# Kernel tuning notes

Measured on AMD Instinct MI355X. Metric: run time of the kernel, lower is better.

Reference implementation:

```python
import jax, jax.numpy as jnp
import numpy as np

JITTER = 0.05  # posterior-covariance jitter (constructor arg `jitter`)
TWO_PI = 2.0 * np.pi


def _local_k(x1, x2, ls, std):
    # 1-D RBF kernel: x1 (A,), x2 (B,) -> (A, B)
    d2 = jnp.square(x1[:, None] - x2[None, :])
    return (std * std) * jnp.exp(-0.5 * d2 / (ls * ls))


def setup_inputs() -> dict:
    key = jax.random.key(0)
    ks = jax.random.split(key, 8)
    N, D, M = 3072, 4, 512
    X = jax.random.normal(ks[0], (N, D), dtype=jnp.float32)
    y = jax.random.normal(ks[1], (N, 1), dtype=jnp.float32)
    X_bar = jax.random.normal(ks[2], (M, D), dtype=jnp.float32)
    # learned parameters (moderate positive values so fp32 Choleskys are stable)
    local_gp_ls = 1.0 + 0.1 * jax.random.normal(ks[3], (D,), dtype=jnp.float32)
    local_gp_std = 0.5 + 0.05 * jax.random.normal(ks[4], (D,), dtype=jnp.float32)
    local_gp_noise_std = 0.3 * jnp.ones((D,), dtype=jnp.float32)
    local_ls = 0.3 + 0.5 * jax.random.uniform(ks[5], (M, D), dtype=jnp.float32)
    global_gp_std = jnp.array([0.7], dtype=jnp.float32)
    global_gp_noise_std = jnp.array([0.5], dtype=jnp.float32)
    return {
        "X": X, "y": y, "X_bar": X_bar,
        "local_gp_ls": local_gp_ls, "local_gp_std": local_gp_std,
        "local_gp_noise_std": local_gp_noise_std, "local_ls": local_ls,
        "global_gp_std": global_gp_std, "global_gp_noise_std": global_gp_noise_std,
    }


def reference(X, y, X_bar, local_gp_ls, local_gp_std, local_gp_noise_std,
              local_ls, global_gp_std, global_gp_noise_std):
    # NSGP.nlml() in training mode.
    N, D = X.shape
    M = X_bar.shape[0]
    dtype = X.dtype
    eyeM = jnp.eye(M, dtype=dtype)
    eyeN = jnp.eye(N, dtype=dtype)
    log_lbar = jnp.log(jnp.abs(local_ls))  # (M, D)

    def per_dim(xb, xd, ls, std, noise, loglb):
        # local GP over inducing points for one input dimension
        k = _local_k(xb, xb, ls, std) + (noise * noise) * eyeM  # (M, M)
        c = jnp.linalg.cholesky(k)
        alpha = jax.scipy.linalg.cho_solve((c, True), loglb[:, None])  # (M, 1)
        kstar = _local_k(xd, xb, ls, std)  # (N, M)
        l = jnp.exp(kstar @ alpha)[:, 0]   # (N,) predicted lengthscales
        kss = _local_k(xd, xd, ls, std)    # (N, N)
        v = jax.scipy.linalg.cho_solve((c, True), kstar.T)  # (M, N)
        kpost = kss - kstar @ v + JITTER * eyeN             # posterior cov
        pc = jnp.linalg.cholesky(kpost)
        Bd = jnp.sum(jnp.log(jnp.diagonal(pc)))
        return l, Bd

    # batch the per-dimension local-GP work across the D input dims
    l_dn, B_d = jax.vmap(per_dim, in_axes=(1, 1, 0, 0, 0, 1))(
        X_bar, X, local_gp_ls, local_gp_std, local_gp_noise_std, log_lbar)
    l = l_dn.T  # (N, D)

    # nonstationary global kernel (Gibbs kernel)
    l1 = l[:, None, :]                    # (N, 1, D)
    l2 = l[None, :, :]                    # (1, N, D)
    lsq = l1 * l1 + l2 * l2               # (N, N, D)
    suffix = jnp.prod(jnp.sqrt(2.0 * l1 * l2 / lsq), axis=2)  # (N, N)
    d2 = jnp.square(X[:, None, :] - X[None, :, :])            # (N, N, D)
    gvar = global_gp_std[0] * global_gp_std[0]
    K = gvar * suffix * jnp.exp(-jnp.sum(d2 / lsq, axis=2))
    K = K + (global_gp_noise_std[0] ** 2) * eyeN

    L = jnp.linalg.cholesky(K)
    alpha = jax.scipy.linalg.cho_solve((L, True), y)  # (N, 1)
    log2pi = jnp.log(jnp.asarray(TWO_PI, dtype))
    A = 0.5 * ((y.T @ alpha)[0, 0]
               + jnp.sum(jnp.log(jnp.diagonal(L)))
               + N * log2pi)
    B = jnp.sum(B_d) + 0.5 * (M * D * log2pi)
    return A + B
```

## Files before the change

kernel.cpp:

```cpp
#include <hip/hip_runtime.h>
#include <math.h>

#define N_   3072
#define D_   4
#define M_   512
#define NPAD 3200
#define NB   128
#define PW   32
#define NBLK (NPAD/NB)
#define MBLK (M_/NB)
#define JITTER_ 0.05f
#define CBORD 32768.0f
#define LTS  132

__device__ void trsm_tile64(float* A, int lda, int row0, int k0, const float* Tinv,
                            float* As, float* Ts, int lt) {
  const int tx = lt & 15, ty = lt >> 4;
  float acc[4][8];
  #pragma unroll
  for (int i = 0; i < 4; ++i)
    #pragma unroll
    for (int u = 0; u < 8; ++u) acc[i][u] = 0.f;
  for (int ks = 0; ks < NB; ks += 32) {
    for (int t = lt; t < 64*8; t += 256) {
      int r = t >> 3, q = t & 7;
      float4 v = *(const float4*)&A[(size_t)(row0 + r)*lda + k0 + ks + q*4];
      As[(q*4+0)*68 + r] = v.x; As[(q*4+1)*68 + r] = v.y;
      As[(q*4+2)*68 + r] = v.z; As[(q*4+3)*68 + r] = v.w;
    }
    for (int t = lt; t < 128*8; t += 256) {
      int c = t >> 3, q = t & 7;
      float4 v = *(const float4*)&Tinv[c*NB + ks + q*4];
      Ts[(q*4+0)*132 + c] = v.x; Ts[(q*4+1)*132 + c] = v.y;
      Ts[(q*4+2)*132 + c] = v.z; Ts[(q*4+3)*132 + c] = v.w;
    }
    __syncthreads();
    #pragma unroll
    for (int kk = 0; kk < 32; ++kk) {
      float a[4], b[8];
      *(float4*)a      = *(const float4*)&As[kk*68 + ty*4];
      *(float4*)&b[0]  = *(const float4*)&Ts[kk*132 + tx*8];
      *(float4*)&b[4]  = *(const float4*)&Ts[kk*132 + tx*8 + 4];
      #pragma unroll
      for (int i = 0; i < 4; ++i)
        #pragma unroll
        for (int u = 0; u < 8; ++u) acc[i][u] += a[i]*b[u];
    }
    __syncthreads();
  }
  #pragma unroll
  for (int i = 0; i < 4; ++i) {
    size_t off = (size_t)(row0 + ty*4 + i)*lda + k0 + tx*8;
    *(float4*)&A[off]     = make_float4(acc[i][0],acc[i][1],acc[i][2],acc[i][3]);
    *(float4*)&A[off + 4] = make_float4(acc[i][4],acc[i][5],acc[i][6],acc[i][7]);
  }
}

__device__ void presub64(const float* A, int lda, int j0, int p0, int sr, int sc,
                         int valid, float* As, float* Bs, float* LT_, int lt) {
  const int tx = lt & 15, ty = lt >> 4;
  float acc[4][4];
  #pragma unroll
  for (int i=0;i<4;++i){acc[i][0]=0.f;acc[i][1]=0.f;acc[i][2]=0.f;acc[i][3]=0.f;}
  for (int ks = 0; ks < NB; ks += 32) {
    __syncthreads();
    if (valid) {
      for (int t = lt; t < 64*8; t += 256) {
        int rr = t >> 3, qq = t & 7;
        float4 v = *(const float4*)&A[(size_t)(j0+sr*64+rr)*lda + p0 + ks + qq*4];
        As[(qq*4+0)*68+rr]=v.x; As[(qq*4+1)*68+rr]=v.y;
        As[(qq*4+2)*68+rr]=v.z; As[(qq*4+3)*68+rr]=v.w;
        float4 w = *(const float4*)&A[(size_t)(j0+sc*64+rr)*lda + p0 + ks + qq*4];
        Bs[(qq*4+0)*68+rr]=w.x; Bs[(qq*4+1)*68+rr]=w.y;
        Bs[(qq*4+2)*68+rr]=w.z; Bs[(qq*4+3)*68+rr]=w.w;
      }
    }
    __syncthreads();
    if (valid) {
      #pragma unroll
      for (int kk = 0; kk < 32; ++kk) {
        float a[4], b[4];
        *(float4*)a = *(const float4*)&As[kk*68 + ty*4];
        *(float4*)b = *(const float4*)&Bs[kk*68 + tx*4];
        #pragma unroll
        for (int i=0;i<4;++i)
          #pragma unroll
          for (int u=0;u<4;++u) acc[i][u] += a[i]*b[u];
      }
    }
  }
  if (valid) {
    #pragma unroll
    for (int i=0;i<4;++i)
      #pragma unroll
      for (int u=0;u<4;++u) {
        int rr = sr*64 + ty*4 + i, cc = sc*64 + tx*4 + u;
        if (cc <= rr) LT_[cc*LTS + rr] -= acc[i][u];
      }
  }
}

__device__ void potrf_duty(float* A, int lda, int b, int presub, int doInv,
                           float* Tinv, float* logsum, int slot, int limit,
                           float* LT_, float* SM_, float* pivd_) {
  const int tid = threadIdx.x;
  const int j0 = b * NB;
  for (int t = tid; t < NB*NB; t += 512) {
    int r = t >> 7, c = t & 127;
    float v = 0.f;
    if (c <= r) v = A[(size_t)(j0+r)*lda + (j0+c)];
    LT_[c*LTS + r] = v;
  }
  if (presub) {
    int half = tid >> 8, lt = tid & 255;
    float* As = SM_ + half*4352; float* Bs = As + 2176;
    const int p0 = j0 - NB;
    presub64(A, lda, j0, p0, half, 0, 1, As, Bs, LT_, lt);
    presub64(A, lda, j0, p0, 1, 1, half==0 ? 1 : 0, As, Bs, LT_, lt);
  }
  __syncthreads();
  #pragma unroll
  for (int p = 0; p < 4; ++p) {
    const int pc0 = p*PW, pc1 = pc0 + PW;
    for (int j = pc0; j < pc1; ++j) {
      float dd = fmaxf(LT_[j*LTS + j], 1e-30f);
      if (tid == 0) pivd_[j] = dd;
      float rd = 1.0f / dd;
      int wn = pc1 - 1 - j;
      for (int t = tid; t < wn*NB; t += 512) {
        int c = j + 1 + (t >> 7);
        int i = t & 127;
        if (i >= c) LT_[c*LTS + i] -= LT_[j*LTS + i] * LT_[j*LTS + c] * rd;
      }
      __syncthreads();
    }
    for (int t = tid; t < PW*NB; t += 512) {
      int jc = pc0 + (t >> 7);
      int i  = t & 127;
      float dd = pivd_[jc];
      if (i > jc)       LT_[jc*LTS + i] *= rsqrtf(dd);
      else if (i == jc) LT_[jc*LTS + i] = sqrtf(dd);
    }
    __syncthreads();
    if (pc1 < NB) {
      const int rem = NB - pc1, g4 = rem >> 2;
      for (int t = tid; t < g4*g4; t += 512) {
        int tr = t / g4, tc = t - tr*g4;
        if (tc > tr) continue;
        int i0 = pc1 + tr*4, c0 = pc1 + tc*4;
        float acc2[4][4];
        #pragma unroll
        for (int i=0;i<4;++i){acc2[i][0]=0.f;acc2[i][1]=0.f;acc2[i][2]=0.f;acc2[i][3]=0.f;}
        #pragma unroll
        for (int jj = 0; jj < PW; ++jj) {
          float av[4], bv[4];
          *(float4*)av = *(const float4*)&LT_[(pc0+jj)*LTS + i0];
          *(float4*)bv = *(const float4*)&LT_[(pc0+jj)*LTS + c0];
          #pragma unroll
          for (int i=0;i<4;++i)
            #pragma unroll
            for (int u=0;u<4;++u) acc2[i][u] += av[i]*bv[u];
        }
        #pragma unroll
        for (int i=0;i<4;++i)
          #pragma unroll
          for (int u=0;u<4;++u) {
            int rr = i0+i, cc = c0+u;
            if (cc <= rr) LT_[cc*LTS + rr] -= acc2[i][u];
          }
      }
      __syncthreads();
    }
  }
  for (int t = tid; t < NB*NB; t += 512) {
    int r = t >> 7, c = t & 127;
    if (c <= r) A[(size_t)(j0+r)*lda + (j0+c)] = LT_[c*LTS + r];
  }
  {
    float lg = 0.f;
    if (tid < NB) {
      int g = j0 + tid;
      if (g < limit) lg = 0.5f * logf(pivd_[tid]);
    }
    for (int o = 32; o; o >>= 1) lg += __shfl_down(lg, o);
    int wv = tid >> 6;
    if ((tid & 63) == 0 && wv < 2) logsum[slot*2 + wv] = lg;
  }
  if (!doInv) return;
  float* Wp = SM_;
  float* Tt = SM_ + 10240;
  for (int t = tid; t < 4*1024; t += 512) {
    int I = t >> 10, e = t & 1023;
    int r = e >> 5, c = e & 31;
    Wp[(I*(I+1)/2 + I)*1024 + e] = (r == c) ? 1.f : 0.f;
  }
  __syncthreads();
  {
    int wI = tid >> 7;
    int lane = tid & 127;
    float* Rb = &Wp[(wI*(wI+1)/2 + wI)*1024];
    for (int j = 0; j < 32; ++j) {
      float dinv = 1.0f / LT_[(wI*32+j)*LTS + (wI*32+j)];
      for (int t = lane; t < 1024; t += 128) {
        int i = t >> 5, c = t & 31;
        if (i > j && c <= j)
          Rb[i*32 + c] -= LT_[(wI*32+j)*LTS + (wI*32+i)] * Rb[j*32 + c] * dinv;
      }
      __syncthreads();
    }
    for (int t = lane; t < 1024; t += 128) {
      int i = t >> 5, c = t & 31;
      if (c <= i) Rb[i*32 + c] *= 1.0f / LT_[(wI*32+i)*LTS + (wI*32+i)];
    }
    __syncthreads();
  }
  #pragma unroll
  for (int dist = 1; dist < 4; ++dist) {
    const int nb = 4 - dist;
    for (int t = tid; t < nb*1024; t += 512) {
      int bb = t >> 10, e = t & 1023;
      int r = e >> 5, c = e & 31;
      int J = bb, I = bb + dist;
      float s = 0.f;
      for (int K = J; K < I; ++K) {
        const float* Wkj = &Wp[(K*(K+1)/2 + J)*1024];
        #pragma unroll
        for (int k = 0; k < 32; ++k)
          s += LT_[(K*32+k)*LTS + (I*32+r)] * Wkj[k*32 + c];
      }
      Tt[bb*1024 + e] = s;
    }
    __syncthreads();
    for (int t = tid; t < nb*1024; t += 512) {
      int bb = t >> 10, e = t & 1023;
      int r = e >> 5, c = e & 31;
      int J = bb, I = bb + dist;
      const float* Wii = &Wp[(I*(I+1)/2 + I)*1024];
      float s = 0.f;
      #pragma unroll
      for (int k = 0; k < 32; ++k)
        s += Wii[r*32 + k] * Tt[bb*1024 + k*32 + c];
      Wp[(I*(I+1)/2 + J)*1024 + e] = -s;
    }
    __syncthreads();
  }
  for (int t = tid; t < NB*32; t += 512) {
    int i = t >> 5, c4 = (t & 31) * 4;
    int I = i >> 5, J = c4 >> 5;
    float4 v;
    if (J <= I) {
      const float* Wij = &Wp[(I*(I+1)/2 + J)*1024 + (i & 31)*32 + (c4 & 31)];
      v = *(const float4*)Wij;
    } else v = make_float4(0.f, 0.f, 0.f, 0.f);
    *(float4*)&Tinv[i*NB + c4] = v;
  }
}

__global__ __launch_bounds__(512, 1)
void k_panel(float* Abase, size_t aStride, int lda, int k, int init, int doInv,
             float* TinvBase, size_t tz, size_t tk,
             float* logsum, int slotBase, int limit, int nblk) {
  __shared__ __align__(16) float LT[128*LTS];
  __shared__ __align__(16) float SM[13312];
  __shared__ float pivd[NB];
  const int z = blockIdx.z;
  float* A = Abase + (size_t)z*aStride;
  float* Tz = TinvBase + (size_t)z*tz;
  const int tid = threadIdx.x;

  if (init) {
    if (blockIdx.x == 0)
      potrf_duty(A, lda, 0, 0, doInv, Tz, logsum, slotBase + z*32, limit,
                 LT, SM, pivd);
    return;
  }
  const int m = nblk - 1 - k;
  const float* TinvK = Tz + (size_t)k*tk;
  int half = tid >> 8, lt = tid & 255;
  float* As = SM + half*6400;
  float* Ts = As + 2176;

  if (blockIdx.x == 0) {
    trsm_tile64(A, lda, (k+1)*NB + half*64, k*NB, TinvK, As, Ts, lt);
    __syncthreads();
    potrf_duty(A, lda, k+1, 1, doInv, Tz + (size_t)(k+1)*tk,
               logsum, slotBase + z*32 + (k+1), limit, LT, SM, pivd);
  } else {
    int t = 2 + (blockIdx.x - 1)*2 + half;
    if (t < 2*m)
      trsm_tile64(A, lda, (k+1)*NB + t*64, k*NB, TinvK, As, Ts, lt);
  }
}

__global__ __launch_bounds__(256)
void k_syrk(float* Abase, size_t aStride, int lda, int kblk) {
  if (blockIdx.y > blockIdx.x) return;
  if (blockIdx.x < 2 && blockIdx.y < 2) return;
  __shared__ float As[32*68];
  __shared__ float Bs[32*68];
  const int tid = threadIdx.x;
  float* A = Abase + (size_t)blockIdx.z * aStride;
  const int k0 = kblk * NB;
  const int row0 = k0 + NB + blockIdx.x * 64;
  const int col0 = k0 + NB + blockIdx.y * 64;
  const int tx = tid & 15, ty = tid >> 4;
  float acc[4][4];
  #pragma unroll
  for (int i=0;i<4;++i) { acc[i][0]=0.f;acc[i][1]=0.f;acc[i][2]=0.f;acc[i][3]=0.f; }
  for (int ks = 0; ks < NB; ks += 32) {
    for (int t = tid; t < 64*8; t += 256) {
      int r = t >> 3, q = t & 7;
      float4 v = *(const float4*)&A[(size_t)(row0 + r)*lda + k0 + ks + q*4];
      As[(q*4+0)*68 + r] = v.x; As[(q*4+1)*68 + r] = v.y;
      As[(q*4+2)*68 + r] = v.z; As[(q*4+3)*68 + r] = v.w;
      float4 w = *(const float4*)&A[(size_t)(col0 + r)*lda + k0 + ks + q*4];
      Bs[(q*4+0)*68 + r] = w.x; Bs[(q*4+1)*68 + r] = w.y;
      Bs[(q*4+2)*68 + r] = w.z; Bs[(q*4+3)*68 + r] = w.w;
    }
    __syncthreads();
    #pragma unroll
    for (int kk = 0; kk < 32; ++kk) {
      float a[4], b[4];
      *(float4*)a = *(const float4*)&As[kk*68 + ty*4];
      *(float4*)b = *(const float4*)&Bs[kk*68 + tx*4];
      #pragma unroll
      for (int i=0;i<4;++i)
        #pragma unroll
        for (int u=0;u<4;++u) acc[i][u] += a[i]*b[u];
    }
    __syncthreads();
  }
  #pragma unroll
  for (int i=0;i<4;++i) {
    size_t off = (size_t)(row0 + ty*4 + i)*lda + col0 + tx*4;
    float4 v = *(const float4*)&A[off];
    v.x -= acc[i][0]; v.y -= acc[i][1]; v.z -= acc[i][2]; v.w -= acc[i][3];
    *(float4*)&A[off] = v;
  }
}

__global__ __launch_bounds__(256)
void k_build_kb(const float* Xbar, const float* lsp, const float* stdp, const float* noisep,
                float* KbBase, size_t kbStride, int dimBase) {
  int z = blockIdx.z, d = dimBase + z;
  float* Kb = KbBase + (size_t)z*kbStride;
  int idx = blockIdx.x*256 + threadIdx.x;
  if (idx >= M_*M_) return;
  int i = idx >> 9, j = idx & 511;
  float ls = lsp[d], sd = stdp[d], nz = noisep[d];
  float df = Xbar[i*D_ + d] - Xbar[j*D_ + d];
  float v = sd*sd*expf(-0.5f*df*df/(ls*ls));
  if (i == j) v += nz*nz;
  Kb[idx] = v;
}

__global__ __launch_bounds__(256)
void k_build_kstar(const float* X, const float* Xbar, const float* lsp, const float* stdp,
                   float* KSBase, size_t ksStride, int dimBase) {
  int z = blockIdx.z, d = dimBase + z;
  float* KS = KSBase + (size_t)z*ksStride;
  int idx = blockIdx.x*256 + threadIdx.x;
  if (idx >= N_*M_) return;
  int i = idx >> 9, j = idx & 511;
  float ls = lsp[d], sd = stdp[d];
  float df = X[i*D_ + d] - Xbar[j*D_ + d];
  KS[idx] = sd*sd*expf(-0.5f*df*df/(ls*ls));
}

__global__ __launch_bounds__(256)
void k_csolve(float* CBase, size_t cStride, const float* KbBase, size_t kbStride,
              const float* TinvKbBase, size_t tkbStride, int J) {
  __shared__ float sm[12672];
  const int tid = threadIdx.x;
  float* C = CBase + (size_t)blockIdx.z*cStride;
  const float* L = KbBase + (size_t)blockIdx.z*kbStride;
  const float* Tinv = TinvKbBase + (size_t)blockIdx.z*tkbStride + (size_t)J*NB*NB;
  const int row0 = blockIdx.x*64;
  const int tx = tid & 15, ty = tid >> 4;
  float* As = sm; float* Ls = sm + 2176;
  float* Xs = sm; float* Ts = sm + 8448;
  float acc[4][8];
  #pragma unroll
  for (int i=0;i<4;++i) {
    const float* p = &C[(size_t)(row0+ty*4+i)*M_ + J*NB + tx*8];
    float4 v0 = *(const float4*)p, v1 = *(const float4*)(p+4);
    acc[i][0]=v0.x; acc[i][1]=v0.y; acc[i][2]=v0.z; acc[i][3]=v0.w;
    acc[i][4]=v1.x; acc[i][5]=v1.y; acc[i][6]=v1.z; acc[i][7]=v1.w;
  }
  for (int P = 0; P < J; ++P) {
    for (int ks = 0; ks < NB; ks += 32) {
      __syncthreads();
      for (int t = tid; t < 64*8; t += 256) {
        int r = t >> 3, q = t & 7;
        float4 v = *(const float4*)&C[(size_t)(row0+r)*M_ + P*NB + ks + q*4];
        As[(q*4+0)*68+r]=v.x; As[(q*4+1)*68+r]=v.y; As[(q*4+2)*68+r]=v.z; As[(q*4+3)*68+r]=v.w;
      }
      for (int t = tid; t < 128*8; t += 256) {
        int c = t >> 3, q = t & 7;
        float4 v = *(const float4*)&L[(size_t)(J*NB+c)*M_ + P*NB + ks + q*4];
        Ls[(q*4+0)*132+c]=v.x; Ls[(q*4+1)*132+c]=v.y; Ls[(q*4+2)*132+c]=v.z; Ls[(q*4+3)*132+c]=v.w;
      }
      __syncthreads();
      #pragma unroll
      for (int kk = 0; kk < 32; ++kk) {
        float a[4], b[8];
        *(float4*)a     = *(const float4*)&As[kk*68 + ty*4];
        *(float4*)&b[0] = *(const float4*)&Ls[kk*132 + tx*8];
        *(float4*)&b[4] = *(const float4*)&Ls[kk*132 + tx*8 + 4];
        #pragma unroll
        for (int i=0;i<4;++i)
          #pragma unroll
          for (int u=0;u<8;++u) acc[i][u] -= a[i]*b[u];
      }
    }
  }
  __syncthreads();
  #pragma unroll
  for (int i=0;i<4;++i)
    #pragma unroll
    for (int u=0;u<8;++u) Xs[(ty*4+i)*132 + tx*8+u] = acc[i][u];
  #pragma unroll
  for (int i=0;i<4;++i)
    #pragma unroll
    for (int u=0;u<8;++u) acc[i][u] = 0.f;
  for (int ms = 0; ms < NB; ms += 32) {
    for (int t = tid; t < 128*8; t += 256) {
      int c = t >> 3, q = t & 7;
      float4 v = *(const float4*)&Tinv[c*NB + ms + q*4];
      Ts[(q*4+0)*132+c]=v.x; Ts[(q*4+1)*132+c]=v.y; Ts[(q*4+2)*132+c]=v.z; Ts[(q*4+3)*132+c]=v.w;
    }
    __syncthreads();
    #pragma unroll
    for (int mm = 0; mm < 32; ++mm) {
      float a[4], b[8];
      a[0]=Xs[(ty*4+0)*132+ms+mm]; a[1]=Xs[(ty*4+1)*132+ms+mm];
      a[2]=Xs[(ty*4+2)*132+ms+mm]; a[3]=Xs[(ty*4+3)*132+ms+mm];
      *(float4*)&b[0] = *(const float4*)&Ts[mm*132 + tx*8];
      *(float4*)&b[4] = *(const float4*)&Ts[mm*132 + tx*8 + 4];
      #pragma unroll
      for (int i=0;i<4;++i)
        #pragma unroll
        for (int u=0;u<8;++u) acc[i][u] += a[i]*b[u];
    }
    __syncthreads();
  }
  #pragma unroll
  for (int i=0;i<4;++i) {
    float* p = &C[(size_t)(row0+ty*4+i)*M_ + J*NB + tx*8];
    *(float4*)p     = make_float4(acc[i][0],acc[i][1],acc[i][2],acc[i][3]);
    *(float4*)(p+4) = make_float4(acc[i][4],acc[i][5],acc[i][6],acc[i][7]);
  }
}

__global__ __launch_bounds__(256)
void k_fwdsub(const float* KbBase, size_t kbStride,
              const float* TkbBase, size_t tkbStride,
              const float* lls, float* wBase, size_t wStride, int dimBase) {
  __shared__ float w[M_];
  __shared__ float tv[NB];
  __shared__ float red[256];
  int z = blockIdx.z, d = dimBase + z;
  const float* L = KbBase + (size_t)z*kbStride;
  const float* Tk = TkbBase + (size_t)z*tkbStride;
  float* wout = wBase + (size_t)z*wStride;
  const int tid = threadIdx.x;
  for (int i = tid; i < M_; i += 256) w[i] = logf(fabsf(lls[i*D_ + d]));
  __syncthreads();
  const int r = tid >> 1, h = tid & 1;
  for (int J = 0; J < 4; ++J) {
    float s = 0.f;
    int half = (J*NB) >> 1;
    for (int k = h*half; k < (h+1)*half; k += 4) {
      float4 lv = *(const float4*)&L[(size_t)(J*NB + r)*M_ + k];
      s += lv.x*w[k] + lv.y*w[k+1] + lv.z*w[k+2] + lv.w*w[k+3];
    }
    red[tid] = s;
    __syncthreads();
    if (h == 0) tv[r] = w[J*NB + r] - red[2*r] - red[2*r+1];
    __syncthreads();
    const float* Ti = Tk + (size_t)J*NB*NB;
    s = 0.f;
    for (int k = h*64; k < h*64 + 64; k += 4) {
      float4 tw = *(const float4*)&Ti[r*NB + k];
      s += tw.x*tv[k] + tw.y*tv[k+1] + tw.z*tv[k+2] + tw.w*tv[k+3];
    }
    red[tid] = s;
    __syncthreads();
    if (h == 0) w[J*NB + r] = red[2*r] + red[2*r+1];
    __syncthreads();
  }
  for (int i = tid; i < M_; i += 256) wout[i] = w[i];
}

__global__ __launch_bounds__(256)
void k_gemv_l(const float* CBase, size_t cStride, const float* wBase, size_t wStride,
              float* lvec, int dimBase) {
  int z = blockIdx.z, d = dimBase + z;
  const float* C = CBase + (size_t)z*cStride;
  const float* w = wBase + (size_t)z*wStride;
  __shared__ float ws[M_];
  for (int i = threadIdx.x; i < M_; i += 256) ws[i] = w[i];
  __syncthreads();
  int wid = threadIdx.x >> 6, lane = threadIdx.x & 63;
  int row = blockIdx.x*4 + wid;
  if (row >= N_) return;
  float s = 0.f;
  const float* cr = &C[(size_t)row*M_];
  for (int k = lane; k < M_; k += 64) s += cr[k]*ws[k];
  for (int o = 32; o; o >>= 1) s += __shfl_down(s, o);
  if (lane == 0) lvec[row*D_ + d] = expf(s);
}

__global__ __launch_bounds__(256)
void k_kpost(const float* X, const float* lsp, const float* stdp,
             const float* CBase, size_t cStride,
             float* Abase, size_t aStride, int dimBase) {
  if (blockIdx.y > blockIdx.x) return;
  __shared__ float As[32*68];
  __shared__ float Bs[32*68];
  int z = blockIdx.z, d = dimBase + z;
  const float* C = CBase + (size_t)z*cStride;
  float* A = Abase + (size_t)z*aStride;
  const int row0 = blockIdx.x*64, col0 = blockIdx.y*64;
  const int tid = threadIdx.x, tx = tid & 15, ty = tid >> 4;
  float acc[4][4];
  #pragma unroll
  for (int i=0;i<4;++i) { acc[i][0]=0.f;acc[i][1]=0.f;acc[i][2]=0.f;acc[i][3]=0.f; }
  if (row0 < N_) {
    for (int ks = 0; ks < M_; ks += 32) {
      for (int t = tid; t < 64*8; t += 256) {
        int r = t >> 3, q = t & 7;
        float4 v = *(const float4*)&C[(size_t)(row0+r)*M_ + ks + q*4];
        As[(q*4+0)*68+r]=v.x; As[(q*4+1)*68+r]=v.y; As[(q*4+2)*68+r]=v.z; As[(q*4+3)*68+r]=v.w;
        float4 w2 = *(const float4*)&C[(size_t)(col0+r)*M_ + ks + q*4];
        Bs[(q*4+0)*68+r]=w2.x; Bs[(q*4+1)*68+r]=w2.y; Bs[(q*4+2)*68+r]=w2.z; Bs[(q*4+3)*68+r]=w2.w;
      }
      __syncthreads();
      #pragma unroll
      for (int kk=0; kk<32; ++kk) {
        float a[4], b[4];
        *(float4*)a = *(const float4*)&As[kk*68 + ty*4];
        *(float4*)b = *(const float4*)&Bs[kk*68 + tx*4];
        #pragma unroll
        for (int i=0;i<4;++i)
          #pragma unroll
          for (int u=0;u<4;++u) acc[i][u] += a[i]*b[u];
      }
      __syncthreads();
    }
  }
  float ls = lsp[d], sd = stdp[d];
  float inv2 = -0.5f/(ls*ls), s2 = sd*sd;
  #pragma unroll
  for (int i=0;i<4;++i) {
    int gi = row0 + ty*4 + i;
    float xi = (gi < N_) ? X[gi*D_ + d] : 0.f;
    #pragma unroll
    for (int u=0;u<4;++u) {
      int gj = col0 + tx*4 + u;
      float v;
      if (gi < N_ && gj < N_) {
        float df = xi - X[gj*D_ + d];
        v = s2*expf(inv2*df*df) - acc[i][u];
        if (gi == gj) v += JITTER_;
      } else {
        v = (gi == gj) ? 1.f : 0.f;
      }
      A[(size_t)gi*NPAD + gj] = v;
    }
  }
}

__global__ __launch_bounds__(256)
void k_kfinal(const float* X, const float* lvec, const float* y,
              const float* gstd, const float* gnoise, float* A) {
  int idx = blockIdx.x*256 + threadIdx.x;
  if (idx >= NPAD*NPAD) return;
  int gi = idx / NPAD, gj = idx - (idx/NPAD)*NPAD;
  float v;
  if (gi < N_ && gj < N_) {
    float gv = gstd[0]*gstd[0];
    float prod = 1.f, s = 0.f;
    #pragma unroll
    for (int d = 0; d < D_; ++d) {
      float l1 = lvec[gi*D_ + d], l2 = lvec[gj*D_ + d];
      float lsq = l1*l1 + l2*l2;
      prod *= 2.f*l1*l2/lsq;
      float df = X[gi*D_ + d] - X[gj*D_ + d];
      s += df*df/lsq;
    }
    v = gv * sqrtf(prod) * expf(-s);
    if (gi == gj) v += gnoise[0]*gnoise[0];
  } else if (gi == N_ && gj < N_) v = y[gj];
  else if (gj == N_ && gi < N_) v = y[gi];
  else if (gi == N_ && gj == N_) v = CBORD;
  else v = (gi == gj) ? 1.f : 0.f;
  A[idx] = v;
}

__global__ void k_finalize(const float* A, const float* logsum, float* out) {
  if (threadIdx.x != 0 || blockIdx.x != 0) return;
  float sumB = 0.f;
  for (int z = 0; z < 4; ++z)
    for (int k = 0; k < NBLK; ++k) {
      int slot = z*32 + k;
      sumB += logsum[slot*2] + logsum[slot*2+1];
    }
  float sumL = 0.f;
  for (int k = 0; k < NBLK; ++k) {
    int slot = 128 + k;
    sumL += logsum[slot*2] + logsum[slot*2+1];
  }
  float lb = A[(size_t)N_*NPAD + N_];
  float yKy = CBORD - lb*lb;
  const float LOG2PI = 1.8378770664093453f;
  float Aterm = 0.5f*(yKy + sumL + (float)N_*LOG2PI);
  float Bterm = sumB + 0.5f*(float)(M_*D_)*LOG2PI;
  out[0] = Aterm + Bterm;
}

static void run_chain(float* A, size_t aS, int lda, int nblk,
                      float* Tinv, size_t tz, size_t tk, int invAll,
                      float* lgs, int slotBase, int limit, int nz,
                      hipStream_t stream) {
  int doInv0 = (invAll || nblk > 1) ? 1 : 0;
  k_panel<<<dim3(1,1,nz),512,0,stream>>>(A,aS,lda, 0,1,doInv0, Tinv,tz,tk,
                                         lgs,slotBase,limit, nblk);
  for (int k = 0; k < nblk-1; ++k) {
    int m = nblk-1-k;
    int doInv = (invAll || (k+1 < nblk-1)) ? 1 : 0;
    k_panel<<<dim3(m,1,nz),512,0,stream>>>(A,aS,lda, k,0,doInv, Tinv,tz,tk,
                                           lgs,slotBase,limit, nblk);
    if (m >= 2)
      k_syrk<<<dim3(2*m,2*m,nz),256,0,stream>>>(A,aS,lda,k);
  }
}

extern "C" void kernel_launch(void* const* d_in, const int* in_sizes, int n_in,
                              void* d_out, int out_size, void* d_ws, size_t ws_size,
                              hipStream_t stream) {
  const float* X    = (const float*)d_in[0];
  const float* y    = (const float*)d_in[1];
  const float* Xbar = (const float*)d_in[2];
  const float* lgls = (const float*)d_in[3];
  const float* lgstd= (const float*)d_in[4];
  const float* lgnz = (const float*)d_in[5];
  const float* lls  = (const float*)d_in[6];
  const float* gstd = (const float*)d_in[7];
  const float* gnz  = (const float*)d_in[8];
  float* out = (float*)d_out;

  const size_t A_SZ   = (size_t)NPAD*NPAD;
  const size_t KS_SZ  = (size_t)N_*M_;
  const size_t KB_SZ  = (size_t)M_*M_;
  const size_t TKB_SZ = (size_t)MBLK*NB*NB;
  const size_t TBG_SZ = (size_t)NBLK*NB*NB;
  const size_t W_SZ   = (size_t)M_;
  const size_t LV_SZ  = (size_t)N_*D_;
  const size_t LOG_SZ = 1024;

  size_t need2 = (5*A_SZ + 4*(KS_SZ + KB_SZ + TKB_SZ + W_SZ) + 5*TBG_SZ
                  + LV_SZ + LOG_SZ + 1024);
  size_t per1  = A_SZ + KS_SZ + KB_SZ + TKB_SZ + TBG_SZ + W_SZ;
  size_t need1 = 4*per1 + LV_SZ + LOG_SZ + 256;

  if (ws_size >= need2 * sizeof(float)) {
    float* p = (float*)d_ws;
    float* A    = p; p += 5*A_SZ;
    float* KS   = p; p += 4*KS_SZ;
    float* Kb   = p; p += 4*KB_SZ;
    float* Tkb  = p; p += 4*TKB_SZ;
    float* Tbig = p; p += 5*TBG_SZ;
    float* wv   = p; p += 4*W_SZ;
    float* lv   = p; p += LV_SZ;
    float* lgs  = p; p += LOG_SZ;

    k_build_kb<<<dim3((M_*M_+255)/256,1,4),256,0,stream>>>(Xbar,lgls,lgstd,lgnz,Kb,KB_SZ,0);
    run_chain(Kb, KB_SZ, M_, MBLK, Tkb, TKB_SZ, (size_t)NB*NB, 1, lgs, 192, 0, 4, stream);
    k_fwdsub<<<dim3(1,1,4),256,0,stream>>>(Kb,KB_SZ,Tkb,TKB_SZ,lls,wv,W_SZ,0);
    k_build_kstar<<<dim3((N_*M_+255)/256,1,4),256,0,stream>>>(X,Xbar,lgls,lgstd,KS,KS_SZ,0);
    for (int J = 0; J < MBLK; ++J)
      k_csolve<<<dim3(N_/64,1,4),256,0,stream>>>(KS,KS_SZ,Kb,KB_SZ,Tkb,TKB_SZ,J);
    k_gemv_l<<<dim3(N_/4,1,4),256,0,stream>>>(KS,KS_SZ,wv,W_SZ,lv,0);
    k_kpost<<<dim3(NPAD/64,NPAD/64,4),256,0,stream>>>(X,lgls,lgstd,KS,KS_SZ,A,A_SZ,0);
    k_kfinal<<<dim3((NPAD*NPAD+255)/256,1,1),256,0,stream>>>(X,lv,y,gstd,gnz,A+4*A_SZ);
    run_chain(A, A_SZ, NPAD, NBLK, Tbig, TBG_SZ, (size_t)NB*NB, 0, lgs, 0, N_, 5, stream);
    k_finalize<<<1,64,0,stream>>>(A+4*A_SZ,lgs,out);
    return;
  }

  bool batched = ws_size >= need1 * sizeof(float);
  int nz = batched ? 4 : 1;
  float* p = (float*)d_ws;
  float* A    = p; p += (size_t)nz*A_SZ;
  float* KS   = p; p += (size_t)nz*KS_SZ;
  float* Kb   = p; p += (size_t)nz*KB_SZ;
  float* Tkb  = p; p += (size_t)nz*TKB_SZ;
  float* Tbig = p; p += (size_t)nz*TBG_SZ;
  float* wv   = p; p += (size_t)nz*W_SZ;
  float* lv   = p; p += LV_SZ;
  float* lgs  = p; p += LOG_SZ;

  int npass = batched ? 1 : 4;
  for (int pass = 0; pass < npass; ++pass) {
    int dimBase  = batched ? 0 : pass;
    int slotBase = batched ? 0 : pass*32;
    k_build_kb<<<dim3((M_*M_+255)/256,1,nz),256,0,stream>>>(Xbar,lgls,lgstd,lgnz,Kb,KB_SZ,dimBase);
    run_chain(Kb, KB_SZ, M_, MBLK, Tkb, TKB_SZ, (size_t)NB*NB, 1, lgs, 192+slotBase, 0, nz, stream);
    k_fwdsub<<<dim3(1,1,nz),256,0,stream>>>(Kb,KB_SZ,Tkb,TKB_SZ,lls,wv,W_SZ,dimBase);
    k_build_kstar<<<dim3((N_*M_+255)/256,1,nz),256,0,stream>>>(X,Xbar,lgls,lgstd,KS,KS_SZ,dimBase);
    for (int J = 0; J < MBLK; ++J)
      k_csolve<<<dim3(N_/64,1,nz),256,0,stream>>>(KS,KS_SZ,Kb,KB_SZ,Tkb,TKB_SZ,J);
    k_gemv_l<<<dim3(N_/4,1,nz),256,0,stream>>>(KS,KS_SZ,wv,W_SZ,lv,dimBase);
    k_kpost<<<dim3(NPAD/64,NPAD/64,nz),256,0,stream>>>(X,lgls,lgstd,KS,KS_SZ,A,A_SZ,dimBase);
    run_chain(A, A_SZ, NPAD, NBLK, Tbig, TBG_SZ, (size_t)NB*NB, 0, lgs, slotBase, N_, nz, stream);
  }
  k_kfinal<<<dim3((NPAD*NPAD+255)/256,1,1),256,0,stream>>>(X,lv,y,gstd,gnz,A);
  run_chain(A, A_SZ, NPAD, NBLK, Tbig, TBG_SZ, (size_t)NB*NB, 0, lgs, 128, N_, 1, stream);
  k_finalize<<<1,64,0,stream>>>(A,lgs,out);
}
```

Baseline: 8.684 ms.

## Fuse panel and trailing SYRK into one lookahead kernel per Cholesky step

Restructures the blocked Cholesky so that each step launches a single combined kernel instead of separate panel and SYRK launches. Block 0 applies the deferred trailing update from the previous step to the next panel, runs its TRSM and factors the diagonal block. The other blocks handle the remaining TRSM tiles and the lagged SYRK tiles, which cuts launches per step and overlaps the critical-path factorization with the bulk update. The diagonal factor now works from a smaller shared-memory strip with 256 threads, reading and writing global memory directly. That trades the large LDS footprint for more global traffic on the serial path, and the triangular-index decode and lagged-update bookkeeping add correctness risk.

```diff
diff --git a/kernel.cpp b/kernel.cpp
--- a/kernel.cpp
+++ b/kernel.cpp
@@ -6,12 +6,48 @@
 #define M_   512
 #define NPAD 3200
 #define NB   128
-#define PW   32
 #define NBLK (NPAD/NB)
 #define MBLK (M_/NB)
 #define JITTER_ 0.05f
 #define CBORD 32768.0f
-#define LTS  132
+
+__device__ void syrk64(float* A, int lda, int gr0, int gc0, int k0,
+                       float* As, float* Bs, int lt) {
+  const int tx = lt & 15, ty = lt >> 4;
+  float acc[4][4];
+  #pragma unroll
+  for (int i=0;i<4;++i){acc[i][0]=0.f;acc[i][1]=0.f;acc[i][2]=0.f;acc[i][3]=0.f;}
+  for (int ks = 0; ks < NB; ks += 32) {
+    __syncthreads();
+    for (int t = lt; t < 64*8; t += 256) {
+      int rr = t >> 3, qq = t & 7;
+      float4 v = *(const float4*)&A[(size_t)(gr0+rr)*lda + k0 + ks + qq*4];
+      As[(qq*4+0)*68+rr]=v.x; As[(qq*4+1)*68+rr]=v.y;
+      As[(qq*4+2)*68+rr]=v.z; As[(qq*4+3)*68+rr]=v.w;
+      float4 w = *(const float4*)&A[(size_t)(gc0+rr)*lda + k0 + ks + qq*4];
+      Bs[(qq*4+0)*68+rr]=w.x; Bs[(qq*4+1)*68+rr]=w.y;
+      Bs[(qq*4+2)*68+rr]=w.z; Bs[(qq*4+3)*68+rr]=w.w;
+    }
+    __syncthreads();
+    #pragma unroll
+    for (int kk = 0; kk < 32; ++kk) {
+      float a[4], b[4];
+      *(float4*)a = *(const float4*)&As[kk*68 + ty*4];
+      *(float4*)b = *(const float4*)&Bs[kk*68 + tx*4];
+      #pragma unroll
+      for (int i=0;i<4;++i)
+        #pragma unroll
+        for (int u=0;u<4;++u) acc[i][u] += a[i]*b[u];
+    }
+  }
+  #pragma unroll
+  for (int i=0;i<4;++i) {
+    size_t off = (size_t)(gr0 + ty*4 + i)*lda + gc0 + tx*4;
+    float4 v = *(const float4*)&A[off];
+    v.x -= acc[i][0]; v.y -= acc[i][1]; v.z -= acc[i][2]; v.w -= acc[i][3];
+    *(float4*)&A[off] = v;
+  }
+}
 
 __device__ void trsm_tile64(float* A, int lda, int row0, int k0, const float* Tinv,
                             float* As, float* Ts, int lt) {
@@ -56,287 +92,218 @@
   }
 }
 
-__device__ void presub64(const float* A, int lda, int j0, int p0, int sr, int sc,
-                         int valid, float* As, float* Bs, float* LT_, int lt) {
-  const int tx = lt & 15, ty = lt >> 4;
-  float acc[4][4];
-  #pragma unroll
-  for (int i=0;i<4;++i){acc[i][0]=0.f;acc[i][1]=0.f;acc[i][2]=0.f;acc[i][3]=0.f;}
-  for (int ks = 0; ks < NB; ks += 32) {
-    __syncthreads();
-    if (valid) {
-      for (int t = lt; t < 64*8; t += 256) {
-        int rr = t >> 3, qq = t & 7;
-        float4 v = *(const float4*)&A[(size_t)(j0+sr*64+rr)*lda + p0 + ks + qq*4];
-        As[(qq*4+0)*68+rr]=v.x; As[(qq*4+1)*68+rr]=v.y;
-        As[(qq*4+2)*68+rr]=v.z; As[(qq*4+3)*68+rr]=v.w;
-        float4 w = *(const float4*)&A[(size_t)(j0+sc*64+rr)*lda + p0 + ks + qq*4];
-        Bs[(qq*4+0)*68+rr]=w.x; Bs[(qq*4+1)*68+rr]=w.y;
-        Bs[(qq*4+2)*68+rr]=w.z; Bs[(qq*4+3)*68+rr]=w.w;
-      }
-    }
-    __syncthreads();
-    if (valid) {
-      #pragma unroll
-      for (int kk = 0; kk < 32; ++kk) {
-        float a[4], b[4];
-        *(float4*)a = *(const float4*)&As[kk*68 + ty*4];
-        *(float4*)b = *(const float4*)&Bs[kk*68 + tx*4];
-        #pragma unroll
-        for (int i=0;i<4;++i)
-          #pragma unroll
-          for (int u=0;u<4;++u) acc[i][u] += a[i]*b[u];
-      }
-    }
-  }
-  if (valid) {
-    #pragma unroll
-    for (int i=0;i<4;++i)
-      #pragma unroll
-      for (int u=0;u<4;++u) {
-        int rr = sr*64 + ty*4 + i, cc = sc*64 + tx*4 + u;
-        if (cc <= rr) LT_[cc*LTS + rr] -= acc[i][u];
-      }
-  }
-}
-
-__device__ void potrf_duty(float* A, int lda, int b, int presub, int doInv,
-                           float* Tinv, float* logsum, int slot, int limit,
-                           float* LT_, float* SM_, float* pivd_) {
+__device__ void b_potrf_l2(float* A, int lda, int dj, float* Tinv, int doInv,
+                           float* logsum, int slot, int limit,
+                           float* SM, float* diagv) {
   const int tid = threadIdx.x;
-  const int j0 = b * NB;
-  for (int t = tid; t < NB*NB; t += 512) {
-    int r = t >> 7, c = t & 127;
-    float v = 0.f;
-    if (c <= r) v = A[(size_t)(j0+r)*lda + (j0+c)];
-    LT_[c*LTS + r] = v;
-  }
-  if (presub) {
-    int half = tid >> 8, lt = tid & 255;
-    float* As = SM_ + half*4352; float* Bs = As + 2176;
-    const int p0 = j0 - NB;
-    presub64(A, lda, j0, p0, half, 0, 1, As, Bs, LT_, lt);
-    presub64(A, lda, j0, p0, 1, 1, half==0 ? 1 : 0, As, Bs, LT_, lt);
-  }
-  __syncthreads();
+  float* Ps = SM;
   #pragma unroll
   for (int p = 0; p < 4; ++p) {
-    const int pc0 = p*PW, pc1 = pc0 + PW;
-    for (int j = pc0; j < pc1; ++j) {
-      float dd = fmaxf(LT_[j*LTS + j], 1e-30f);
-      if (tid == 0) pivd_[j] = dd;
-      float rd = 1.0f / dd;
-      int wn = pc1 - 1 - j;
-      for (int t = tid; t < wn*NB; t += 512) {
-        int c = j + 1 + (t >> 7);
-        int i = t & 127;
-        if (i >= c) LT_[c*LTS + i] -= LT_[j*LTS + i] * LT_[j*LTS + c] * rd;
-      }
-      __syncthreads();
-    }
-    for (int t = tid; t < PW*NB; t += 512) {
-      int jc = pc0 + (t >> 7);
-      int i  = t & 127;
-      float dd = pivd_[jc];
-      if (i > jc)       LT_[jc*LTS + i] *= rsqrtf(dd);
-      else if (i == jc) LT_[jc*LTS + i] = sqrtf(dd);
-    }
-    __syncthreads();
-    if (pc1 < NB) {
-      const int rem = NB - pc1, g4 = rem >> 2;
-      for (int t = tid; t < g4*g4; t += 512) {
+    const int pc0 = p*32;
+    const int nr = NB - pc0;
+    __syncthreads();
+    for (int t = tid; t < nr*32; t += 256) {
+      int r2 = t >> 5, c2 = t & 31;
+      Ps[r2*33 + c2] = A[(size_t)(dj+pc0+r2)*lda + dj+pc0+c2];
+    }
+    __syncthreads();
+    for (int j = 0; j < 32; ++j) {
+      if (tid == 0) {
+        float piv = sqrtf(fmaxf(Ps[j*33+j], 1e-30f));
+        Ps[j*33+j] = piv;
+        diagv[pc0+j] = piv;
+      }
+      __syncthreads();
+      float ip = 1.0f / Ps[j*33+j];
+      for (int t = tid; t < nr-1-j; t += 256)
+        Ps[(j+1+t)*33 + j] *= ip;
+      __syncthreads();
+      int rw = nr-1-j, cw = 31-j;
+      for (int t = tid; t < rw*cw; t += 256) {
+        int rr = t / cw, cc2 = t - rr*cw;
+        int i = j+1+rr, c2 = j+1+cc2;
+        Ps[i*33 + c2] -= Ps[i*33 + j] * Ps[c2*33 + j];
+      }
+      __syncthreads();
+    }
+    for (int t = tid; t < nr*32; t += 256) {
+      int r2 = t >> 5, c2 = t & 31;
+      if (r2 >= c2)
+        A[(size_t)(dj+pc0+r2)*lda + dj+pc0+c2] = Ps[r2*33 + c2];
+    }
+    __syncthreads();
+    if (p < 3) {
+      int rem = nr - 32;
+      int g4 = rem >> 2;
+      for (int t = tid; t < g4*g4; t += 256) {
         int tr = t / g4, tc = t - tr*g4;
         if (tc > tr) continue;
-        int i0 = pc1 + tr*4, c0 = pc1 + tc*4;
-        float acc2[4][4];
-        #pragma unroll
-        for (int i=0;i<4;++i){acc2[i][0]=0.f;acc2[i][1]=0.f;acc2[i][2]=0.f;acc2[i][3]=0.f;}
-        #pragma unroll
-        for (int jj = 0; jj < PW; ++jj) {
+        int i0 = 32 + tr*4, c0 = 32 + tc*4;
+        float acc[4][4];
+        #pragma unroll
+        for (int i=0;i<4;++i){acc[i][0]=0.f;acc[i][1]=0.f;acc[i][2]=0.f;acc[i][3]=0.f;}
+        #pragma unroll
+        for (int jj = 0; jj < 32; ++jj) {
           float av[4], bv[4];
-          *(float4*)av = *(const float4*)&LT_[(pc0+jj)*LTS + i0];
-          *(float4*)bv = *(const float4*)&LT_[(pc0+jj)*LTS + c0];
+          #pragma unroll
+          for (int x=0;x<4;++x) { av[x] = Ps[(i0+x)*33+jj]; bv[x] = Ps[(c0+x)*33+jj]; }
           #pragma unroll
           for (int i=0;i<4;++i)
             #pragma unroll
-            for (int u=0;u<4;++u) acc2[i][u] += av[i]*bv[u];
+            for (int u=0;u<4;++u) acc[i][u] += av[i]*bv[u];
         }
         #pragma unroll
         for (int i=0;i<4;++i)
           #pragma unroll
           for (int u=0;u<4;++u) {
             int rr = i0+i, cc = c0+u;
-            if (cc <= rr) LT_[cc*LTS + rr] -= acc2[i][u];
+            if (cc <= rr)
+              A[(size_t)(dj+pc0+rr)*lda + dj+pc0+cc] -= acc[i][u];
           }
       }
       __syncthreads();
     }
-  }
-  for (int t = tid; t < NB*NB; t += 512) {
-    int r = t >> 7, c = t & 127;
-    if (c <= r) A[(size_t)(j0+r)*lda + (j0+c)] = LT_[c*LTS + r];
   }
   {
     float lg = 0.f;
     if (tid < NB) {
-      int g = j0 + tid;
-      if (g < limit) lg = 0.5f * logf(pivd_[tid]);
+      int g = dj + tid;
+      if (g < limit) lg = logf(diagv[tid]);
     }
     for (int o = 32; o; o >>= 1) lg += __shfl_down(lg, o);
     int wv = tid >> 6;
     if ((tid & 63) == 0 && wv < 2) logsum[slot*2 + wv] = lg;
   }
   if (!doInv) return;
-  float* Wp = SM_;
-  float* Tt = SM_ + 10240;
-  for (int t = tid; t < 4*1024; t += 512) {
-    int I = t >> 10, e = t & 1023;
-    int r = e >> 5, c = e & 31;
-    Wp[(I*(I+1)/2 + I)*1024 + e] = (r == c) ? 1.f : 0.f;
-  }
+  float* Wd = SM;
+  float* Tt = SM + 4224;
   __syncthreads();
   {
-    int wI = tid >> 7;
-    int lane = tid & 127;
-    float* Rb = &Wp[(wI*(wI+1)/2 + wI)*1024];
+    int w = tid >> 6, lane = tid & 63;
+    float* R = Wd + w*1056;
+    for (int t = lane; t < 1024; t += 64) {
+      int i=t>>5, c2=t&31; R[i*33+c2] = (i==c2)?1.f:0.f;
+    }
+    __syncthreads();
     for (int j = 0; j < 32; ++j) {
-      float dinv = 1.0f / LT_[(wI*32+j)*LTS + (wI*32+j)];
-      for (int t = lane; t < 1024; t += 128) {
-        int i = t >> 5, c = t & 31;
-        if (i > j && c <= j)
-          Rb[i*32 + c] -= LT_[(wI*32+j)*LTS + (wI*32+i)] * Rb[j*32 + c] * dinv;
-      }
-      __syncthreads();
-    }
-    for (int t = lane; t < 1024; t += 128) {
-      int i = t >> 5, c = t & 31;
-      if (c <= i) Rb[i*32 + c] *= 1.0f / LT_[(wI*32+i)*LTS + (wI*32+i)];
-    }
-    __syncthreads();
-  }
-  #pragma unroll
-  for (int dist = 1; dist < 4; ++dist) {
-    const int nb = 4 - dist;
-    for (int t = tid; t < nb*1024; t += 512) {
-      int bb = t >> 10, e = t & 1023;
-      int r = e >> 5, c = e & 31;
-      int J = bb, I = bb + dist;
-      float s = 0.f;
-      for (int K = J; K < I; ++K) {
-        const float* Wkj = &Wp[(K*(K+1)/2 + J)*1024];
-        #pragma unroll
-        for (int k = 0; k < 32; ++k)
-          s += LT_[(K*32+k)*LTS + (I*32+r)] * Wkj[k*32 + c];
-      }
-      Tt[bb*1024 + e] = s;
-    }
-    __syncthreads();
-    for (int t = tid; t < nb*1024; t += 512) {
-      int bb = t >> 10, e = t & 1023;
-      int r = e >> 5, c = e & 31;
-      int J = bb, I = bb + dist;
-      const float* Wii = &Wp[(I*(I+1)/2 + I)*1024];
-      float s = 0.f;
-      #pragma unroll
-      for (int k = 0; k < 32; ++k)
-        s += Wii[r*32 + k] * Tt[bb*1024 + k*32 + c];
-      Wp[(I*(I+1)/2 + J)*1024 + e] = -s;
-    }
-    __syncthreads();
-  }
-  for (int t = tid; t < NB*32; t += 512) {
-    int i = t >> 5, c4 = (t & 31) * 4;
-    int I = i >> 5, J = c4 >> 5;
-    float4 v;
-    if (J <= I) {
-      const float* Wij = &Wp[(I*(I+1)/2 + J)*1024 + (i & 31)*32 + (c4 & 31)];
-      v = *(const float4*)Wij;
-    } else v = make_float4(0.f, 0.f, 0.f, 0.f);
-    *(float4*)&Tinv[i*NB + c4] = v;
-  }
-}
-
-__global__ __launch_bounds__(512, 1)
-void k_panel(float* Abase, size_t aStride, int lda, int k, int init, int doInv,
+      float dinv = 1.0f / A[(size_t)(dj+w*32+j)*lda + dj+w*32+j];
+      for (int t = lane; t < 1024; t += 64) {
+        int i = t>>5, c2 = t&31;
+        if (i > j && c2 <= j)
+          R[i*33+c2] -= A[(size_t)(dj+w*32+i)*lda + dj+w*32+j] * R[j*33+c2] * dinv;
+      }
+      __syncthreads();
+    }
+    for (int t = lane; t < 1024; t += 64) {
+      int i=t>>5, c2=t&31;
+      if (c2 <= i) R[i*33+c2] *= 1.0f / A[(size_t)(dj+w*32+i)*lda + dj+w*32+i];
+    }
+    __syncthreads();
+  }
+  for (int t = tid; t < NB*NB; t += 256) {
+    int i = t >> 7, c2 = t & 127;
+    int I = i >> 5, J = c2 >> 5;
+    float v = 0.f;
+    if (I == J) v = Wd[I*1056 + (i&31)*33 + (c2&31)];
+    Tinv[i*NB + c2] = v;
+  }
+  __syncthreads();
+  for (int d = 1; d < 4; ++d) {
+    for (int J = 0; J + d < 4; ++J) {
+      int I = J + d;
+      for (int t = tid; t < 1024; t += 256) {
+        int r2 = t >> 5, c2 = t & 31;
+        float s = 0.f;
+        for (int K = J; K < I; ++K) {
+          const float* Arow = &A[(size_t)(dj+I*32+r2)*lda + dj + K*32];
+          const float* Wcol = &Tinv[(size_t)(K*32)*NB + J*32 + c2];
+          #pragma unroll
+          for (int kk2 = 0; kk2 < 32; ++kk2)
+            s += Arow[kk2] * Wcol[(size_t)kk2*NB];
+        }
+        Tt[r2*33 + c2] = s;
+      }
+      __syncthreads();
+      for (int t = tid; t < 1024; t += 256) {
+        int r2 = t >> 5, c2 = t & 31;
+        float s = 0.f;
+        #pragma unroll
+        for (int kk2 = 0; kk2 < 32; ++kk2)
+          s += Wd[I*1056 + r2*33 + kk2] * Tt[kk2*33 + c2];
+        Tinv[(size_t)(I*32+r2)*NB + J*32 + c2] = -s;
+      }
+      __syncthreads();
+    }
+  }
+}
+
+__global__ __launch_bounds__(256)
+void k_init(float* Abase, size_t aStride, int lda, float* TinvBase, size_t tz,
+            float* logsum, int slotBase, int limit, int doInv) {
+  __shared__ __align__(16) float SM[6528];
+  __shared__ float diagv[NB];
+  int z = blockIdx.z;
+  b_potrf_l2(Abase + (size_t)z*aStride, lda, 0, TinvBase + (size_t)z*tz, doInv,
+             logsum, slotBase + z*32, limit, SM, diagv);
+}
+
+__global__ __launch_bounds__(256)
+void k_combo(float* Abase, size_t aStride, int lda, int k, int doInv,
              float* TinvBase, size_t tz, size_t tk,
-             float* logsum, int slotBase, int limit, int nblk) {
-  __shared__ __align__(16) float LT[128*LTS];
-  __shared__ __align__(16) float SM[13312];
-  __shared__ float pivd[NB];
+             float* logsum, int slotBase, int limit, int nP) {
+  __shared__ __align__(16) float SM[6528];
+  __shared__ float diagv[NB];
   const int z = blockIdx.z;
   float* A = Abase + (size_t)z*aStride;
   float* Tz = TinvBase + (size_t)z*tz;
   const int tid = threadIdx.x;
-
-  if (init) {
-    if (blockIdx.x == 0)
-      potrf_duty(A, lda, 0, 0, doInv, Tz, logsum, slotBase + z*32, limit,
-                 LT, SM, pivd);
+  const int b = blockIdx.x;
+  const int kNB = k*NB, dj = kNB + NB;
+  const float* TinvK = Tz + (size_t)k*tk;
+
+  if (b == 0) {
+    if (k >= 1) {
+      syrk64(A, lda, dj,    kNB,    (k-1)*NB, SM, SM+2176, tid);
+      syrk64(A, lda, dj+64, kNB,    (k-1)*NB, SM, SM+2176, tid);
+      syrk64(A, lda, dj,    kNB+64, (k-1)*NB, SM, SM+2176, tid);
+      syrk64(A, lda, dj+64, kNB+64, (k-1)*NB, SM, SM+2176, tid);
+    }
+    __syncthreads();
+    trsm_tile64(A, lda, dj,    kNB, TinvK, SM, SM+2176, tid);
+    __syncthreads();
+    trsm_tile64(A, lda, dj+64, kNB, TinvK, SM, SM+2176, tid);
+    __syncthreads();
+    if (k >= 1) {
+      syrk64(A, lda, dj,    dj,    (k-1)*NB, SM, SM+2176, tid);
+      syrk64(A, lda, dj+64, dj,    (k-1)*NB, SM, SM+2176, tid);
+      syrk64(A, lda, dj+64, dj+64, (k-1)*NB, SM, SM+2176, tid);
+    }
+    syrk64(A, lda, dj,    dj,    kNB, SM, SM+2176, tid);
+    syrk64(A, lda, dj+64, dj,    kNB, SM, SM+2176, tid);
+    syrk64(A, lda, dj+64, dj+64, kNB, SM, SM+2176, tid);
+    __syncthreads();
+    b_potrf_l2(A, lda, dj, Tz + (size_t)(k+1)*tk, doInv,
+               logsum, slotBase + z*32 + (k+1), limit, SM, diagv);
     return;
   }
-  const int m = nblk - 1 - k;
-  const float* TinvK = Tz + (size_t)k*tk;
-  int half = tid >> 8, lt = tid & 255;
-  float* As = SM + half*6400;
-  float* Ts = As + 2176;
-
-  if (blockIdx.x == 0) {
-    trsm_tile64(A, lda, (k+1)*NB + half*64, k*NB, TinvK, As, Ts, lt);
-    __syncthreads();
-    potrf_duty(A, lda, k+1, 1, doInv, Tz + (size_t)(k+1)*tk,
-               logsum, slotBase + z*32 + (k+1), limit, LT, SM, pivd);
-  } else {
-    int t = 2 + (blockIdx.x - 1)*2 + half;
-    if (t < 2*m)
-      trsm_tile64(A, lda, (k+1)*NB + t*64, k*NB, TinvK, As, Ts, lt);
-  }
-}
-
-__global__ __launch_bounds__(256)
-void k_syrk(float* Abase, size_t aStride, int lda, int kblk) {
-  if (blockIdx.y > blockIdx.x) return;
-  if (blockIdx.x < 2 && blockIdx.y < 2) return;
-  __shared__ float As[32*68];
-  __shared__ float Bs[32*68];
-  const int tid = threadIdx.x;
-  float* A = Abase + (size_t)blockIdx.z * aStride;
-  const int k0 = kblk * NB;
-  const int row0 = k0 + NB + blockIdx.x * 64;
-  const int col0 = k0 + NB + blockIdx.y * 64;
-  const int tx = tid & 15, ty = tid >> 4;
-  float acc[4][4];
-  #pragma unroll
-  for (int i=0;i<4;++i) { acc[i][0]=0.f;acc[i][1]=0.f;acc[i][2]=0.f;acc[i][3]=0.f; }
-  for (int ks = 0; ks < NB; ks += 32) {
-    for (int t = tid; t < 64*8; t += 256) {
-      int r = t >> 3, q = t & 7;
-      float4 v = *(const float4*)&A[(size_t)(row0 + r)*lda + k0 + ks + q*4];
-      As[(q*4+0)*68 + r] = v.x; As[(q*4+1)*68 + r] = v.y;
-      As[(q*4+2)*68 + r] = v.z; As[(q*4+3)*68 + r] = v.w;
-      float4 w = *(const float4*)&A[(size_t)(col0 + r)*lda + k0 + ks + q*4];
-      Bs[(q*4+0)*68 + r] = w.x; Bs[(q*4+1)*68 + r] = w.y;
-      Bs[(q*4+2)*68 + r] = w.z; Bs[(q*4+3)*68 + r] = w.w;
-    }
-    __syncthreads();
-    #pragma unroll
-    for (int kk = 0; kk < 32; ++kk) {
-      float a[4], b[4];
-      *(float4*)a = *(const float4*)&As[kk*68 + ty*4];
-      *(float4*)b = *(const float4*)&Bs[kk*68 + tx*4];
-      #pragma unroll
-      for (int i=0;i<4;++i)
-        #pragma unroll
-        for (int u=0;u<4;++u) acc[i][u] += a[i]*b[u];
-    }
-    __syncthreads();
-  }
-  #pragma unroll
-  for (int i=0;i<4;++i) {
-    size_t off = (size_t)(row0 + ty*4 + i)*lda + col0 + tx*4;
-    float4 v = *(const float4*)&A[off];
-    v.x -= acc[i][0]; v.y -= acc[i][1]; v.z -= acc[i][2]; v.w -= acc[i][3];
-    *(float4*)&A[off] = v;
-  }
+  if (b <= nP) {
+    int t64 = (b-1) + 2;
+    int row0 = dj + t64*64;
+    if (k >= 1) {
+      syrk64(A, lda, row0, kNB,    (k-1)*NB, SM, SM+2176, tid);
+      syrk64(A, lda, row0, kNB+64, (k-1)*NB, SM, SM+2176, tid);
+    }
+    __syncthreads();
+    trsm_tile64(A, lda, row0, kNB, TinvK, SM, SM+2176, tid);
+    return;
+  }
+  int s = b - 1 - nP;
+  int idxp = s + 3;
+  int r = (int)((sqrtf(8.f*(float)idxp + 1.f) - 1.f)*0.5f);
+  while ((r+1)*(r+2)/2 <= idxp) ++r;
+  while (r*(r+1)/2 > idxp) --r;
+  int c = idxp - r*(r+1)/2;
+  syrk64(A, lda, dj + r*64, dj + c*64, (k-1)*NB, SM, SM+2176, tid);
 }
 
 __global__ __launch_bounds__(256)
@@ -624,15 +591,14 @@
                       float* lgs, int slotBase, int limit, int nz,
                       hipStream_t stream) {
   int doInv0 = (invAll || nblk > 1) ? 1 : 0;
-  k_panel<<<dim3(1,1,nz),512,0,stream>>>(A,aS,lda, 0,1,doInv0, Tinv,tz,tk,
-                                         lgs,slotBase,limit, nblk);
+  k_init<<<dim3(1,1,nz),256,0,stream>>>(A,aS,lda,Tinv,tz,lgs,slotBase,limit,doInv0);
   for (int k = 0; k < nblk-1; ++k) {
     int m = nblk-1-k;
+    int nP = (m >= 2) ? 2*(m-1) : 0;
+    int nS = (k >= 1) ? (m*(2*m+1) - 3) : 0;
     int doInv = (invAll || (k+1 < nblk-1)) ? 1 : 0;
-    k_panel<<<dim3(m,1,nz),512,0,stream>>>(A,aS,lda, k,0,doInv, Tinv,tz,tk,
-                                           lgs,slotBase,limit, nblk);
-    if (m >= 2)
-      k_syrk<<<dim3(2*m,2*m,nz),256,0,stream>>>(A,aS,lda,k);
+    k_combo<<<dim3(1+nP+nS,1,nz),256,0,stream>>>(A,aS,lda,k,doInv,Tinv,tz,tk,
+                                                 lgs,slotBase,limit,nP);
   }
 }
 
```

Result: slower. 11.98 ms, median of 2 (+37.9%).
